# Performance work log

Measured on AMD Instinct MI355X. Metric: run time of the kernel, lower is better.

Reference implementation:

```python
import jax, jax.numpy as jnp
import numpy as np

S, D = 8192, 2048      # sequence length, feature dim (input_size)
H, E, K, L = 64, 64, 2, 64  # gate hidden, expert count, top-k, expert layer_size
EPS = 1e-12            # torch F.normalize eps


def setup_inputs() -> dict:
    key = jax.random.key(0)
    ks = jax.random.split(key, 5)
    x = jax.random.normal(ks[0], (S, D), dtype=jnp.float32)
    # torch nn.Linear weights have shape [out_features, in_features]
    Wg_in = jax.random.normal(ks[1], (H, D), dtype=jnp.float32) * 0.02   # gate.input
    Wg_lin = jax.random.normal(ks[2], (E, H), dtype=jnp.float32) * 0.02  # gate.linear
    Wg_out = jax.random.normal(ks[3], (1, S), dtype=jnp.float32) * 0.02  # gate.output
    We = jax.random.normal(ks[4], (E, L, D), dtype=jnp.float32) * 0.02   # expert weight bank
    return {"x": x, "Wg_in": Wg_in, "Wg_lin": Wg_lin, "Wg_out": Wg_out, "We": We}


def reference(x, Wg_in, Wg_lin, Wg_out, We):
    # --- SparseGate (eval mode: dropout = identity) ---
    h = x @ Wg_in.T                         # [S, H]
    logits = h @ Wg_lin.T                   # [S, E]
    scores = (logits.T @ Wg_out.T)[:, 0]    # Linear(S,1) applied to [E,S] -> [E]
    topv, idx = jax.lax.top_k(scores, K)    # global top-k experts for whole input
    g = jax.nn.softmax(topv)                # softmax over the k selected logits

    # --- dispatch to k selected experts (FFNN: Linear -> normalize(-1) -> GELU) ---
    Wsel = We[idx]                          # [K, L, D]
    z = jnp.einsum('sd,kld->ksl', x, Wsel)  # [K, S, L]
    z = z / jnp.maximum(jnp.linalg.norm(z, axis=-1, keepdims=True), EPS)
    z = jax.nn.gelu(z, approximate=False)   # torch GELU default is exact erf

    # --- weighted combine: sum_k g_k * expert_k(x) ---
    return jnp.einsum('k,ksl->sl', g, z)    # [S, L]
```

## Files before the change

### kernel.cpp

```cpp
#include <hip/hip_runtime.h>
#include <hip/hip_bf16.h>
#include <math.h>

#define D_DIM 2048
#define L_DIM 64
#define E_NUM 64
#define H_DIM 64

typedef float f32x4_t __attribute__((ext_vector_type(4)));
typedef __bf16 bf16x8_t __attribute__((ext_vector_type(8)));

#define WS_UPART 0u
#define WS_U     (128u * 2048u * 4u)
#define WS_V     (WS_U + 2048u * 4u)
#define WS_META  (WS_V + 256u)
#define WS_WB    (WS_META + 64u)
#define WS_PART  (WS_WB + 128u * 2048u * 2u)


__global__ void k_upart(const float* __restrict__ x, const float* __restrict__ wout,
                        float* __restrict__ upart) {
  const int d4 = (blockIdx.x * 256 + threadIdx.x) * 4;
  const int s0 = blockIdx.y * 64;
  const float* xp = x + (size_t)s0 * D_DIM + d4;
  float4 acc = make_float4(0.f, 0.f, 0.f, 0.f);
#pragma unroll 8
  for (int i = 0; i < 64; ++i) {
    const float w = wout[s0 + i];
    const float4 xv = *reinterpret_cast<const float4*>(xp + (size_t)i * D_DIM);
    acc.x += xv.x * w; acc.y += xv.y * w; acc.z += xv.z * w; acc.w += xv.w * w;
  }
  *reinterpret_cast<float4*>(upart + (size_t)blockIdx.y * D_DIM + d4) = acc;
}

__global__ void k_ufinish(const float* __restrict__ upart, float* __restrict__ u) {
  const int d = blockIdx.x * 256 + threadIdx.x;
  float s = 0.f;
#pragma unroll 8
  for (int c = 0; c < 128; ++c) s += upart[(size_t)c * D_DIM + d];
  u[d] = s;
}

__global__ void k_v(const float* __restrict__ wg_in, const float* __restrict__ u,
                    float* __restrict__ v) {
  const int h = blockIdx.x;
  const int t = threadIdx.x;
  const float4* wr = reinterpret_cast<const float4*>(wg_in + (size_t)h * D_DIM);
  const float4* ur = reinterpret_cast<const float4*>(u);
  float s = 0.f;
#pragma unroll
  for (int i = t; i < 512; i += 256) {
    const float4 a = wr[i];
    const float4 b = ur[i];
    s += a.x * b.x + a.y * b.y + a.z * b.z + a.w * b.w;
  }
  __shared__ float red[4];
#pragma unroll
  for (int off = 32; off; off >>= 1) s += __shfl_down(s, off, 64);
  if ((t & 63) == 0) red[t >> 6] = s;
  __syncthreads();
  if (t == 0) v[h] = red[0] + red[1] + red[2] + red[3];
}

__global__ void k_gate(const float* __restrict__ wg_lin, const float* __restrict__ v,
                       int* __restrict__ sel, float* __restrict__ g) {
  __shared__ float vv[H_DIM];
  __shared__ float sc[E_NUM];
  const int t = threadIdx.x;
  vv[t] = v[t];
  __syncthreads();
  float s = 0.f;
#pragma unroll 8
  for (int hh = 0; hh < H_DIM; ++hh) s += wg_lin[t * H_DIM + hh] * vv[hh];
  sc[t] = s;
  __syncthreads();
  if (t == 0) {
    int b1 = 0; float m1 = sc[0];
    for (int e = 1; e < E_NUM; ++e) { if (sc[e] > m1) { m1 = sc[e]; b1 = e; } }
    int b2 = -1; float m2 = -3.4e38f;
    for (int e = 0; e < E_NUM; ++e) {
      if (e != b1 && sc[e] > m2) { m2 = sc[e]; b2 = e; }
    }
    const float e2 = expf(m2 - m1);
    const float g0 = 1.0f / (1.0f + e2);
    sel[0] = b1; sel[1] = b2;
    g[0] = g0; g[1] = 1.0f - g0;
  }
}

__global__ void k_wb(const float* __restrict__ we, const int* __restrict__ sel,
                     __hip_bfloat16* __restrict__ wbt) {
  const int n = blockIdx.x;
  const int e = sel[n >> 6];
  const int l = n & 63;
  const float* src = we + ((size_t)e * L_DIM + l) * D_DIM;
  const int t = threadIdx.x;
  const int d8 = t * 8;
  const int kstep = d8 >> 6;
  const int kc = (d8 >> 3) & 7;
  const float4 a = reinterpret_cast<const float4*>(src)[2 * t];
  const float4 b = reinterpret_cast<const float4*>(src)[2 * t + 1];
  union { __hip_bfloat16 h[8]; uint4 u; } pk;
  pk.h[0] = __float2bfloat16(a.x); pk.h[1] = __float2bfloat16(a.y);
  pk.h[2] = __float2bfloat16(a.z); pk.h[3] = __float2bfloat16(a.w);
  pk.h[4] = __float2bfloat16(b.x); pk.h[5] = __float2bfloat16(b.y);
  pk.h[6] = __float2bfloat16(b.z); pk.h[7] = __float2bfloat16(b.w);
  const size_t off = (size_t)kstep * 8192 + n * 64 + ((kc ^ (n & 7)) * 8);
  *reinterpret_cast<uint4*>(wbt + off) = pk.u;
}

__device__ __forceinline__ void async_ld16(const void* gp, void* lp) {
  __builtin_amdgcn_global_load_lds(
      (const __attribute__((address_space(1))) unsigned int*)gp,
      (__attribute__((address_space(3))) unsigned int*)lp, 16, 0, 0);
}

__device__ __forceinline__ float gelu_f(float v) {
  return 0.5f * v * (1.0f + erff(v * 0.70710678118654752440f));
}

__global__ __launch_bounds__(256, 4) void k_moe_gemm(
    const float* __restrict__ x, const __hip_bfloat16* __restrict__ wbt,
    float* __restrict__ part) {
  __shared__ __align__(16) unsigned char lds[64 * 144 + 16384];
  unsigned char* ldsA = lds;
  unsigned char* ldsB = lds + 64 * 144;

  const int tid = threadIdx.x;
  const int w = tid >> 6, lane = tid & 63;
  const int wm = w >> 1, wn = w & 1;
  const int mb = blockIdx.x;
  const int kg = blockIdx.y;
  const int fr = lane & 15, fq = lane >> 4;
  const int m0 = mb * 64;

  f32x4_t acc[2][4];
#pragma unroll
  for (int mf = 0; mf < 2; ++mf)
#pragma unroll
    for (int nf = 0; nf < 4; ++nf) acc[mf][nf] = (f32x4_t){0.f, 0.f, 0.f, 0.f};

  for (int kk = 0; kk < 4; ++kk) {
    const int kstep = kg * 4 + kk;
    const int k0 = kstep * 64;
    if (kk) __syncthreads();
#pragma unroll
    for (int ph = 0; ph < 4; ++ph) {
      const int c = ph * 256 + tid;
      async_ld16(wbt + (size_t)kstep * 8192 + c * 8, ldsB + c * 16);
    }
#pragma unroll
    for (int ph = 0; ph < 2; ++ph) {
      const int c = ph * 256 + tid;
      const int r = c >> 3, c8 = (c & 7) * 8;
      const float* gp = x + (size_t)(m0 + r) * D_DIM + k0 + c8;
      const float4 a0 = *reinterpret_cast<const float4*>(gp);
      const float4 a1 = *reinterpret_cast<const float4*>(gp + 4);
      union { __hip_bfloat16 h[8]; uint4 u; } pk;
      pk.h[0] = __float2bfloat16(a0.x); pk.h[1] = __float2bfloat16(a0.y);
      pk.h[2] = __float2bfloat16(a0.z); pk.h[3] = __float2bfloat16(a0.w);
      pk.h[4] = __float2bfloat16(a1.x); pk.h[5] = __float2bfloat16(a1.y);
      pk.h[6] = __float2bfloat16(a1.z); pk.h[7] = __float2bfloat16(a1.w);
      *reinterpret_cast<uint4*>(ldsA + r * 144 + c8 * 2) = pk.u;
    }
    __syncthreads();
    union fragu { uint4 u; bf16x8_t v; };
    fragu af[2][2], bf_[4][2];
#pragma unroll
    for (int mf = 0; mf < 2; ++mf)
#pragma unroll
      for (int ks = 0; ks < 2; ++ks) {
        const int ar = wm * 32 + mf * 16 + fr;
        af[mf][ks].u = *reinterpret_cast<const uint4*>(
            ldsA + ar * 144 + (ks * 4 + fq) * 16);
      }
#pragma unroll
    for (int nf = 0; nf < 4; ++nf)
#pragma unroll
      for (int ks = 0; ks < 2; ++ks) {
        const int br = wn * 64 + nf * 16 + fr;
        const int kq = ks * 4 + fq;
        bf_[nf][ks].u = *reinterpret_cast<const uint4*>(
            ldsB + br * 128 + ((kq ^ (br & 7)) * 16));
      }
#pragma unroll
    for (int mf = 0; mf < 2; ++mf)
#pragma unroll
      for (int nf = 0; nf < 4; ++nf) {
        acc[mf][nf] = __builtin_amdgcn_mfma_f32_16x16x32_bf16(
            af[mf][0].v, bf_[nf][0].v, acc[mf][nf], 0, 0, 0);
        acc[mf][nf] = __builtin_amdgcn_mfma_f32_16x16x32_bf16(
            af[mf][1].v, bf_[nf][1].v, acc[mf][nf], 0, 0, 0);
      }
  }

#pragma unroll
  for (int mf = 0; mf < 2; ++mf)
#pragma unroll
    for (int nf = 0; nf < 4; ++nf)
#pragma unroll
      for (int reg = 0; reg < 4; ++reg) {
        const int r = m0 + wm * 32 + mf * 16 + fq * 4 + reg;
        const int c = wn * 64 + nf * 16 + fr;
        part[((size_t)kg * 8192 + r) * 128 + c] = acc[mf][nf][reg];
      }
}

__global__ __launch_bounds__(256) void k_finish(const float* __restrict__ part,
                                                const float* __restrict__ gw,
                                                float* __restrict__ out) {
  __shared__ float z[32 * 132];
  __shared__ float ps[32 * 8];
  const int tid = threadIdx.x;
  const int m0 = blockIdx.x * 32;
  const float g0 = gw[0], g1 = gw[1];
  const size_t KSTRIDE = (size_t)8192 * 128;
#pragma unroll
  for (int p = 0; p < 4; ++p) {
    const int idx = p * 256 + tid;
    const int r = idx >> 5, c4 = (idx & 31) * 4;
    const float* pp = part + ((size_t)(m0 + r)) * 128 + c4;
    f32x4_t s = (f32x4_t){0.f, 0.f, 0.f, 0.f};
#pragma unroll
    for (int kgi = 0; kgi < 8; ++kgi)
      s = s + *reinterpret_cast<const f32x4_t*>(pp + kgi * KSTRIDE);
    z[r * 132 + c4 + 0] = s[0];
    z[r * 132 + c4 + 1] = s[1];
    z[r * 132 + c4 + 2] = s[2];
    z[r * 132 + c4 + 3] = s[3];
  }
  __syncthreads();
  {
    const int r = tid >> 3, seg = tid & 7;
    float s = 0.f;
#pragma unroll
    for (int i2 = 0; i2 < 16; ++i2) {
      const float t2 = z[r * 132 + seg * 16 + i2];
      s += t2 * t2;
    }
    ps[r * 8 + seg] = s;
  }
  __syncthreads();
  {
    const int r = tid >> 3, j = tid & 7;
    const float s0 = ps[r * 8 + 0] + ps[r * 8 + 1] + ps[r * 8 + 2] + ps[r * 8 + 3];
    const float s1 = ps[r * 8 + 4] + ps[r * 8 + 5] + ps[r * 8 + 6] + ps[r * 8 + 7];
    const float i0 = 1.0f / fmaxf(sqrtf(s0), 1e-12f);
    const float i1 = 1.0f / fmaxf(sqrtf(s1), 1e-12f);
    float o[8];
#pragma unroll
    for (int i2 = 0; i2 < 8; ++i2) {
      const int c = j * 8 + i2;
      const float za = z[r * 132 + c] * i0;
      const float zb2 = z[r * 132 + 64 + c] * i1;
      o[i2] = g0 * gelu_f(za) + g1 * gelu_f(zb2);
    }
    float4* op = reinterpret_cast<float4*>(out + (size_t)(m0 + r) * 64 + j * 8);
    op[0] = make_float4(o[0], o[1], o[2], o[3]);
    op[1] = make_float4(o[4], o[5], o[6], o[7]);
  }
}

extern "C" void kernel_launch(void* const* d_in, const int* in_sizes, int n_in,
                              void* d_out, int out_size, void* d_ws, size_t ws_size,
                              hipStream_t stream) {
  (void)in_sizes; (void)n_in; (void)out_size; (void)ws_size;
  const float* x      = (const float*)d_in[0];
  const float* wg_in  = (const float*)d_in[1];
  const float* wg_lin = (const float*)d_in[2];
  const float* wg_out = (const float*)d_in[3];
  const float* we     = (const float*)d_in[4];
  float* out = (float*)d_out;
  char* ws = (char*)d_ws;

  float* upart = (float*)(ws + WS_UPART);
  float* u     = (float*)(ws + WS_U);
  float* v     = (float*)(ws + WS_V);
  int*   sel   = (int*)(ws + WS_META);
  float* g     = (float*)(ws + WS_META + 8);
  __hip_bfloat16* wbt = (__hip_bfloat16*)(ws + WS_WB);
  float* part = (float*)(ws + WS_PART);

  k_upart  <<<dim3(2, 128), 256, 0, stream>>>(x, wg_out, upart);
  k_ufinish<<<8, 256, 0, stream>>>(upart, u);
  k_v      <<<64, 256, 0, stream>>>(wg_in, u, v);
  k_gate   <<<1, 64, 0, stream>>>(wg_lin, v, sel, g);
  k_wb     <<<128, 256, 0, stream>>>(we, sel, wbt);
  k_moe_gemm<<<dim3(128, 8), 256, 0, stream>>>(x, wbt, part);
  k_finish <<<256, 256, 0, stream>>>(part, g, out);
}
```

Baseline: 160.4 us.

## Double-buffer B tile and prefetch A into registers in MoE GEMM

```diff
diff --git a/kernel.cpp b/kernel.cpp
--- a/kernel.cpp
+++ b/kernel.cpp
@@ -122,9 +122,8 @@
 __global__ __launch_bounds__(256, 4) void k_moe_gemm(
     const float* __restrict__ x, const __hip_bfloat16* __restrict__ wbt,
     float* __restrict__ part) {
-  __shared__ __align__(16) unsigned char lds[64 * 144 + 16384];
-  unsigned char* ldsA = lds;
-  unsigned char* ldsB = lds + 64 * 144;
+  __shared__ __align__(16) unsigned char ldsA[8192];
+  __shared__ __align__(16) unsigned char ldsB[2][16384];
 
   const int tid = threadIdx.x;
   const int w = tid >> 6, lane = tid & 63;
@@ -134,45 +133,62 @@
   const int fr = lane & 15, fq = lane >> 4;
   const int m0 = mb * 64;
 
+  const int c0 = tid, c1 = 256 + tid;
+  const int r0_ = c0 >> 3, kc0 = c0 & 7, r1_ = c1 >> 3, kc1 = c1 & 7;
+  unsigned char* aw0 = ldsA + r0_ * 128 + ((kc0 ^ (r0_ & 7)) << 4);
+  unsigned char* aw1 = ldsA + r1_ * 128 + ((kc1 ^ (r1_ & 7)) << 4);
+  const float* gA0 = x + (size_t)(m0 + r0_) * D_DIM + kc0 * 8;
+  const float* gA1 = x + (size_t)(m0 + r1_) * D_DIM + kc1 * 8;
+
   f32x4_t acc[2][4];
 #pragma unroll
   for (int mf = 0; mf < 2; ++mf)
 #pragma unroll
     for (int nf = 0; nf < 4; ++nf) acc[mf][nf] = (f32x4_t){0.f, 0.f, 0.f, 0.f};
 
-  for (int kk = 0; kk < 4; ++kk) {
-    const int kstep = kg * 4 + kk;
-    const int k0 = kstep * 64;
-    if (kk) __syncthreads();
+  union { __hip_bfloat16 h[8]; uint4 u; } pk;
+  float4 ar[4];
+
+  auto cvt_write = [&]() {
+    pk.h[0] = __float2bfloat16(ar[0].x); pk.h[1] = __float2bfloat16(ar[0].y);
+    pk.h[2] = __float2bfloat16(ar[0].z); pk.h[3] = __float2bfloat16(ar[0].w);
+    pk.h[4] = __float2bfloat16(ar[1].x); pk.h[5] = __float2bfloat16(ar[1].y);
+    pk.h[6] = __float2bfloat16(ar[1].z); pk.h[7] = __float2bfloat16(ar[1].w);
+    *reinterpret_cast<uint4*>(aw0) = pk.u;
+    pk.h[0] = __float2bfloat16(ar[2].x); pk.h[1] = __float2bfloat16(ar[2].y);
+    pk.h[2] = __float2bfloat16(ar[2].z); pk.h[3] = __float2bfloat16(ar[2].w);
+    pk.h[4] = __float2bfloat16(ar[3].x); pk.h[5] = __float2bfloat16(ar[3].y);
+    pk.h[6] = __float2bfloat16(ar[3].z); pk.h[7] = __float2bfloat16(ar[3].w);
+    *reinterpret_cast<uint4*>(aw1) = pk.u;
+  };
+
+  {
+    const int k0 = (kg * 4) * 64;
+    ar[0] = *reinterpret_cast<const float4*>(gA0 + k0);
+    ar[1] = *reinterpret_cast<const float4*>(gA0 + k0 + 4);
+    ar[2] = *reinterpret_cast<const float4*>(gA1 + k0);
+    ar[3] = *reinterpret_cast<const float4*>(gA1 + k0 + 4);
 #pragma unroll
     for (int ph = 0; ph < 4; ++ph) {
       const int c = ph * 256 + tid;
-      async_ld16(wbt + (size_t)kstep * 8192 + c * 8, ldsB + c * 16);
-    }
-#pragma unroll
-    for (int ph = 0; ph < 2; ++ph) {
-      const int c = ph * 256 + tid;
-      const int r = c >> 3, c8 = (c & 7) * 8;
-      const float* gp = x + (size_t)(m0 + r) * D_DIM + k0 + c8;
-      const float4 a0 = *reinterpret_cast<const float4*>(gp);
-      const float4 a1 = *reinterpret_cast<const float4*>(gp + 4);
-      union { __hip_bfloat16 h[8]; uint4 u; } pk;
-      pk.h[0] = __float2bfloat16(a0.x); pk.h[1] = __float2bfloat16(a0.y);
-      pk.h[2] = __float2bfloat16(a0.z); pk.h[3] = __float2bfloat16(a0.w);
-      pk.h[4] = __float2bfloat16(a1.x); pk.h[5] = __float2bfloat16(a1.y);
-      pk.h[6] = __float2bfloat16(a1.z); pk.h[7] = __float2bfloat16(a1.w);
-      *reinterpret_cast<uint4*>(ldsA + r * 144 + c8 * 2) = pk.u;
-    }
+      async_ld16(wbt + (size_t)(kg * 4) * 8192 + c * 8, &ldsB[0][c * 16]);
+    }
+    cvt_write();
     __syncthreads();
+  }
+
+  for (int kk = 0; kk < 4; ++kk) {
+    const int cur = kk & 1;
     union fragu { uint4 u; bf16x8_t v; };
     fragu af[2][2], bf_[4][2];
 #pragma unroll
     for (int mf = 0; mf < 2; ++mf)
 #pragma unroll
       for (int ks = 0; ks < 2; ++ks) {
-        const int ar = wm * 32 + mf * 16 + fr;
+        const int arr = wm * 32 + mf * 16 + fr;
+        const int kq = ks * 4 + fq;
         af[mf][ks].u = *reinterpret_cast<const uint4*>(
-            ldsA + ar * 144 + (ks * 4 + fq) * 16);
+            ldsA + arr * 128 + ((kq ^ (arr & 7)) * 16));
       }
 #pragma unroll
     for (int nf = 0; nf < 4; ++nf)
@@ -181,8 +197,23 @@
         const int br = wn * 64 + nf * 16 + fr;
         const int kq = ks * 4 + fq;
         bf_[nf][ks].u = *reinterpret_cast<const uint4*>(
-            ldsB + br * 128 + ((kq ^ (br & 7)) * 16));
-      }
+            ldsB[cur] + br * 128 + ((kq ^ (br & 7)) * 16));
+      }
+    if (kk < 3) {
+      const int k0n = (kg * 4 + kk + 1) * 64;
+      ar[0] = *reinterpret_cast<const float4*>(gA0 + k0n);
+      ar[1] = *reinterpret_cast<const float4*>(gA0 + k0n + 4);
+      ar[2] = *reinterpret_cast<const float4*>(gA1 + k0n);
+      ar[3] = *reinterpret_cast<const float4*>(gA1 + k0n + 4);
+      __builtin_amdgcn_sched_barrier(0);
+#pragma unroll
+      for (int ph = 0; ph < 4; ++ph) {
+        const int c = ph * 256 + tid;
+        async_ld16(wbt + (size_t)(kg * 4 + kk + 1) * 8192 + c * 8,
+                   &ldsB[cur ^ 1][c * 16]);
+      }
+      __builtin_amdgcn_sched_barrier(0);
+    }
 #pragma unroll
     for (int mf = 0; mf < 2; ++mf)
 #pragma unroll
@@ -192,6 +223,15 @@
         acc[mf][nf] = __builtin_amdgcn_mfma_f32_16x16x32_bf16(
             af[mf][1].v, bf_[nf][1].v, acc[mf][nf], 0, 0, 0);
       }
+    asm volatile("s_waitcnt lgkmcnt(0)" ::: "memory");
+    __builtin_amdgcn_s_barrier();
+    __builtin_amdgcn_sched_barrier(0);
+    if (kk < 3) {
+      cvt_write();
+    }
+    asm volatile("s_waitcnt vmcnt(0) lgkmcnt(0)" ::: "memory");
+    __builtin_amdgcn_s_barrier();
+    __builtin_amdgcn_sched_barrier(0);
   }
 
 #pragma unroll
```

New measurement: 159.3 us. No clear change (-0.6%).
